# Kernel optimization log

Measured on AMD Instinct MI355X. Metric: run time of the kernel, lower is better.

The kernel has to match this reference:

```python
import jax, jax.numpy as jnp
import numpy as np

HEADS = 16
EPS = 1e-12


def setup_inputs() -> dict:
    key = jax.random.key(0)
    ks = jax.random.split(key, 5)
    B, S, H = 4, 2048, 1024
    scale = 1.0 / np.sqrt(H)
    return {
        "input": jax.random.normal(ks[0], (B, S, H), jnp.float32),
        "input_mask": jnp.zeros((B, 1, 1, S), jnp.float32),  # additive mask
        "norm_w": jnp.ones((H,), jnp.float32),
        "norm_b": jnp.zeros((H,), jnp.float32),
        "attn_qkvw": jax.random.normal(ks[1], (3 * H, H), jnp.float32) * scale,
        "attn_qkvb": jax.random.normal(ks[2], (3 * H,), jnp.float32) * 0.01,
        "attn_ow": jax.random.normal(ks[3], (H, H), jnp.float32) * scale,
    }


def reference(input, input_mask, norm_w, norm_b, attn_qkvw, attn_qkvb, attn_ow):
    B, S, H = input.shape
    d_head = H // HEADS

    # qkv_gemm: fused LayerNorm + QKV projection (pre_layer_norm path)
    mu = jnp.mean(input, axis=-1, keepdims=True)
    var = jnp.mean(jnp.square(input - mu), axis=-1, keepdims=True)
    ln = (input - mu) * jax.lax.rsqrt(var + EPS) * norm_w + norm_b
    qkv = ln @ attn_qkvw.T + attn_qkvb  # [B,S,3H]

    q, k, v = jnp.split(qkv, 3, axis=-1)  # each [B,S,H]
    key_layer, value_layer = k, v  # returned pre-transpose, as in the fused path

    qh = q.reshape(B, S, HEADS, d_head).transpose(0, 2, 1, 3)  # [B,h,S,d]
    kh = k.reshape(B, S, HEADS, d_head).transpose(0, 2, 1, 3)
    vh = v.reshape(B, S, HEADS, d_head).transpose(0, 2, 1, 3)

    # fused softmax-attention: score scale nets to 1/sqrt(d_head)
    scores = jnp.einsum("bhqd,bhkd->bhqk", qh, kh) / jnp.sqrt(
        jnp.asarray(d_head, input.dtype)) + input_mask
    p = jax.nn.softmax(scores, axis=-1)
    ctx = jnp.einsum("bhqk,bhkd->bhqd", p, vh)  # [B,h,S,d]
    context_layer = ctx.transpose(0, 2, 1, 3).reshape(B, S, H)

    # vector_matmul output projection (bias added outside this module)
    output = context_layer @ attn_ow.T
    return (output, key_layer, value_layer, context_layer)
```

## Files before the change

### kernel.cpp

```cpp
#include <hip/hip_runtime.h>
#include <cstdint>


typedef __attribute__((ext_vector_type(8))) short short8;
typedef __attribute__((ext_vector_type(4))) short short4v;
typedef __attribute__((ext_vector_type(4))) float floatx4;

#define BSH 8388608
#define PART_STRIDE 8388608
#define LOG2E 1.4426950408889634f

static __device__ __forceinline__ short f2bf(float f) {
  union { float f; uint32_t u; } v; v.f = f;
  uint32_t r = v.u + 0x7fffu + ((v.u >> 16) & 1u);
  return (short)(r >> 16);
}

typedef __attribute__((address_space(1))) void gas_t;
typedef __attribute__((address_space(3))) void las_t;
static __device__ __forceinline__ void async16(const void* g, const void* l) {
  __builtin_amdgcn_global_load_lds((gas_t*)(uintptr_t)g,
                                   (las_t*)(uint32_t)(uintptr_t)l, 16, 0, 0);
}

static __device__ __forceinline__ uint32_t cvt_pk_bf16(float a, float b) {
  uint32_t r;
  asm("v_cvt_pk_bf16_f32 %0, %1, %2" : "=v"(r) : "v"(a), "v"(b));
  return r;
}
static __device__ __forceinline__ void swap32(uint32_t& a, uint32_t& b) {
  asm("v_permlane32_swap_b32 %0, %1" : "+v"(a), "+v"(b));
}
static __device__ __forceinline__ void swap16(uint32_t& a, uint32_t& b) {
  asm("v_permlane16_swap_b32 %0, %1" : "+v"(a), "+v"(b));
}
static __device__ __forceinline__ short8 s8_from(uint32_t a, uint32_t b,
                                                 uint32_t c, uint32_t d) {
  union { uint32_t u[4]; short8 s; } t;
  t.u[0] = a; t.u[1] = b; t.u[2] = c; t.u[3] = d;
  return t.s;
}

__global__ __launch_bounds__(256) void k_convert(const float4* __restrict__ wqkv,
                                                 const float4* __restrict__ ow,
                                                 short4v* __restrict__ dq,
                                                 short4v* __restrict__ dow) {
  const int n1 = (3072 * 1024) / 4, n2 = (1024 * 1024) / 4;
  for (int i = blockIdx.x * 256 + threadIdx.x; i < n1 + n2; i += gridDim.x * 256) {
    float4 v = (i < n1) ? wqkv[i] : ow[i - n1];
    short4v s;
    s[0] = f2bf(v.x); s[1] = f2bf(v.y); s[2] = f2bf(v.z); s[3] = f2bf(v.w);
    if (i < n1) dq[i] = s; else dow[i - n1] = s;
  }
}

__global__ __launch_bounds__(256) void k_ln(const float* __restrict__ x,
                                            const float* __restrict__ w,
                                            const float* __restrict__ bb,
                                            short* __restrict__ out) {
  const int row = blockIdx.x, t = threadIdx.x;
  float4 v = ((const float4*)(x + row * 1024))[t];
  float s = v.x + v.y + v.z + v.w;
  float sq = v.x * v.x + v.y * v.y + v.z * v.z + v.w * v.w;
#pragma unroll
  for (int off = 32; off; off >>= 1) { s += __shfl_down(s, off); sq += __shfl_down(sq, off); }
  __shared__ float ls[4], lq[4];
  if ((t & 63) == 0) { ls[t >> 6] = s; lq[t >> 6] = sq; }
  __syncthreads();
  s = ls[0] + ls[1] + ls[2] + ls[3];
  sq = lq[0] + lq[1] + lq[2] + lq[3];
  float mu = s * (1.0f / 1024.0f);
  float var = sq * (1.0f / 1024.0f) - mu * mu;
  float rs = rsqrtf(fmaxf(var, 0.0f) + 1e-12f);
  float4 wv = ((const float4*)w)[t];
  float4 bv = ((const float4*)bb)[t];
  short4v o;
  o[0] = f2bf((v.x - mu) * rs * wv.x + bv.x);
  o[1] = f2bf((v.y - mu) * rs * wv.y + bv.y);
  o[2] = f2bf((v.z - mu) * rs * wv.z + bv.z);
  o[3] = f2bf((v.w - mu) * rs * wv.w + bv.w);
  ((short4v*)out)[row * 256 + t] = o;
}

template <int MODE>
__global__ __launch_bounds__(256) void k_gemm(const short* __restrict__ A,
                                              const short* __restrict__ Bm,
                                              const float* __restrict__ bias,
                                              float* __restrict__ out,
                                              short* __restrict__ qkvh,
                                              int K, int N) {
  __shared__ short As[128 * 32], Bs[128 * 32];
  const int tid = threadIdx.x, lane = tid & 63, w = tid >> 6;
  const int quad = lane >> 4, l15 = lane & 15;
  const int wr = w >> 1, wc = w & 1;
  const int m0 = blockIdx.y * 128, n0 = blockIdx.x * 128;
  floatx4 acc[4][4] = {};
  for (int k0 = 0; k0 < K; k0 += 32) {
    __syncthreads();
#pragma unroll
    for (int r = 0; r < 2; r++) {
      int pb = r * 256 + w * 64;
      int p = pb + lane;
      int row = p >> 2, c = (p & 3) ^ ((p >> 3) & 3);
      async16(&A[(m0 + row) * K + k0 + c * 8], &As[pb * 8]);
      async16(&Bm[(n0 + row) * K + k0 + c * 8], &Bs[pb * 8]);
    }
    __syncthreads();
    short8 af[4], bf[4];
#pragma unroll
    for (int i = 0; i < 4; i++) {
      int ar = wr * 64 + i * 16 + l15;
      af[i] = *(const short8*)&As[ar * 32 + ((quad ^ ((ar >> 1) & 3)) * 8)];
      int br = wc * 64 + i * 16 + l15;
      bf[i] = *(const short8*)&Bs[br * 32 + ((quad ^ ((br >> 1) & 3)) * 8)];
    }
#pragma unroll
    for (int i = 0; i < 4; i++)
#pragma unroll
      for (int j = 0; j < 4; j++)
        acc[i][j] = __builtin_amdgcn_mfma_f32_16x16x32_bf16(af[i], bf[j], acc[i][j], 0, 0, 0);
  }
  const int grB = m0 + wr * 64, gcB = n0 + wc * 64;
  const float QS = 0.125f * LOG2E;
#pragma unroll
  for (int i = 0; i < 4; i++) {
#pragma unroll
    for (int j = 0; j < 4; j++) {
      int gc = gcB + j * 16 + l15;
      if (MODE == 0) {
        float bv = bias[gc];
        int part = gc >> 10, within = gc & 1023;
        int head = within >> 6, dd = within & 63;
#pragma unroll
        for (int reg = 0; reg < 4; reg++) {
          int gr = grB + i * 16 + quad * 4 + reg;
          float val = acc[i][j][reg] + bv;
          int b_ = gr >> 11, s_ = gr & 2047;
          int hs = (b_ * 16 + head);
          if (part == 0) {
            qkvh[(hs * 2048 + s_) * 64 + dd] = f2bf(val * QS);
          } else if (part == 1) {
            qkvh[PART_STRIDE + (hs * 2048 + s_) * 64 + dd] = f2bf(val);
            out[BSH + gr * 1024 + within] = val;
          } else {
            out[2 * BSH + gr * 1024 + within] = val;
          }
        }
      } else {
#pragma unroll
        for (int reg = 0; reg < 4; reg++) {
          int gr = grB + i * 16 + quad * 4 + reg;
          out[gr * N + gc] = acc[i][j][reg];
        }
      }
    }
  }
}

__global__ __launch_bounds__(256) void k_vt(const float* __restrict__ vsrc,
                                            short* __restrict__ vt) {
  const int st = blockIdx.x, h = blockIdx.y, b = blockIdx.z;
  const int t = threadIdx.x;
  __shared__ short Ls[64 * 64];
  const int s0 = st * 64;
#pragma unroll
  for (int j = 0; j < 4; j++) {
    int flat = j * 1024 + t * 4;
    int sl = flat >> 6, d = flat & 63;
    float4 v4 = *(const float4*)&vsrc[(size_t)(b * 2048 + s0 + sl) * 1024 + h * 64 + d];
    short4v s4;
    s4[0] = f2bf(v4.x); s4[1] = f2bf(v4.y); s4[2] = f2bf(v4.z); s4[3] = f2bf(v4.w);
    *(short4v*)&Ls[sl * 64 + (((d >> 3) ^ (sl & 7)) * 8) + (d & 7)] = s4;
  }
  __syncthreads();
  const int d = t >> 2, sbase = (t & 3) * 16;
#pragma unroll
  for (int half = 0; half < 2; half++) {
    short8 o;
#pragma unroll
    for (int j = 0; j < 8; j++) {
      int s = sbase + half * 8 + j;
      o[j] = Ls[s * 64 + (((d >> 3) ^ (s & 7)) * 8) + (d & 7)];
    }
    *(short8*)&vt[(size_t)((b * 16 + h) * 64 + d) * 2048 + s0 + sbase + half * 8] = o;
  }
}

__global__ __launch_bounds__(256, 4) void k_attn(const short* __restrict__ qkvh,
                                                 const float* __restrict__ mask,
                                                 float* __restrict__ ctx_out,
                                                 short* __restrict__ ctx_bf) {
  const int bid = blockIdx.x;
  const int wid = (bid & 7) * 128 + (bid >> 3);
  const int qt = wid & 15, h = (wid >> 4) & 15, b = wid >> 8;
  const int tid = threadIdx.x, lane = tid & 63, w = tid >> 6;
  const int quad = lane >> 4, l15 = lane & 15;
  __shared__ short Ks[2][64 * 64];
  __shared__ short Vt[2][64 * 64];
  const short* qg = qkvh + (size_t)(b * 16 + h) * 2048 * 64;
  const short* kg = qg + PART_STRIDE;
  const short* vg = qkvh + 2 * PART_STRIDE + (size_t)(b * 16 + h) * 64 * 2048;
  const float* mb = mask + b * 2048;

  short8 qf[2][2];
#pragma unroll
  for (int rt = 0; rt < 2; rt++) {
    const int qr = qt * 128 + w * 32 + rt * 16 + l15;
#pragma unroll
    for (int ks = 0; ks < 2; ks++)
      qf[rt][ks] = *(const short8*)&qg[qr * 64 + ks * 32 + quad * 8];
  }

  short8 ones;
#pragma unroll
  for (int j = 0; j < 8; j++) ones[j] = (short)0x3F80;

  floatx4 accO[2][4] = {};
  floatx4 accL[2] = {};

  auto stage = [&](int kt, int bi) {
#pragma unroll
    for (int r = 0; r < 2; r++) {
      int pb = r * 256 + w * 64;
      int p = pb + lane;
      int row = p >> 3, c = (p & 7) ^ (row & 7);
      async16(&kg[(kt * 64 + row) * 64 + c * 8], &Ks[bi][pb * 8]);
      async16(&vg[row * 2048 + kt * 64 + c * 8], &Vt[bi][pb * 8]);
    }
  };
  stage(0, 0);

  for (int kt = 0; kt < 32; kt++) {
    const int cur = kt & 1;
    __syncthreads();
    if (kt + 1 < 32) stage(kt + 1, cur ^ 1);

    float mv[4][4];
#pragma unroll
    for (int nt = 0; nt < 4; nt++) {
      float4 t = *(const float4*)&mb[kt * 64 + nt * 16 + quad * 4];
      mv[nt][0] = t.x; mv[nt][1] = t.y; mv[nt][2] = t.z; mv[nt][3] = t.w;
    }

    floatx4 sc[2][4] = {};
#pragma unroll
    for (int nt = 0; nt < 4; nt++) {
      const int krow = nt * 16 + l15;
#pragma unroll
      for (int ks = 0; ks < 2; ks++) {
        short8 kf = *(const short8*)&Ks[cur][krow * 64 + (((ks * 4 + quad) ^ (krow & 7)) * 8)];
        sc[0][nt] = __builtin_amdgcn_mfma_f32_16x16x32_bf16(kf, qf[0][ks], sc[0][nt], 0, 0, 0);
        sc[1][nt] = __builtin_amdgcn_mfma_f32_16x16x32_bf16(kf, qf[1][ks], sc[1][nt], 0, 0, 0);
      }
    }

    uint32_t pa[2][2][4];
#pragma unroll
    for (int rt = 0; rt < 2; rt++) {
#pragma unroll
      for (int e = 0; e < 2; e++) {
#pragma unroll
        for (int d = 0; d < 2; d++) {
          float p0 = __builtin_amdgcn_exp2f(fmaf(mv[2 * e][2 * d], LOG2E, sc[rt][2 * e][2 * d]));
          float p1 = __builtin_amdgcn_exp2f(fmaf(mv[2 * e][2 * d + 1], LOG2E, sc[rt][2 * e][2 * d + 1]));
          float p2 = __builtin_amdgcn_exp2f(fmaf(mv[2 * e + 1][2 * d], LOG2E, sc[rt][2 * e + 1][2 * d]));
          float p3 = __builtin_amdgcn_exp2f(fmaf(mv[2 * e + 1][2 * d + 1], LOG2E, sc[rt][2 * e + 1][2 * d + 1]));
          uint32_t rE = cvt_pk_bf16(p0, p1);
          uint32_t rO = cvt_pk_bf16(p2, p3);
          swap32(rE, rO);
          swap16(rE, rO);
          pa[rt][e][d] = rE;
          pa[rt][e][2 + d] = rO;
        }
      }
    }

#pragma unroll
    for (int ks2 = 0; ks2 < 2; ks2++) {
      short8 pf0 = s8_from(pa[0][ks2][0], pa[0][ks2][1], pa[0][ks2][2], pa[0][ks2][3]);
      short8 pf1 = s8_from(pa[1][ks2][0], pa[1][ks2][1], pa[1][ks2][2], pa[1][ks2][3]);
      accL[0] = __builtin_amdgcn_mfma_f32_16x16x32_bf16(pf0, ones, accL[0], 0, 0, 0);
      accL[1] = __builtin_amdgcn_mfma_f32_16x16x32_bf16(pf1, ones, accL[1], 0, 0, 0);
#pragma unroll
      for (int nt2 = 0; nt2 < 4; nt2++) {
        const int vrow = nt2 * 16 + l15;
        short8 vf = *(const short8*)&Vt[cur][vrow * 64 + (((ks2 * 4 + quad) ^ (vrow & 7)) * 8)];
        accO[0][nt2] = __builtin_amdgcn_mfma_f32_16x16x32_bf16(pf0, vf, accO[0][nt2], 0, 0, 0);
        accO[1][nt2] = __builtin_amdgcn_mfma_f32_16x16x32_bf16(pf1, vf, accO[1][nt2], 0, 0, 0);
      }
    }
  }

#pragma unroll
  for (int rt = 0; rt < 2; rt++) {
    float inv[4];
#pragma unroll
    for (int reg = 0; reg < 4; reg++) inv[reg] = 1.0f / accL[rt][reg];
#pragma unroll
    for (int nt2 = 0; nt2 < 4; nt2++)
#pragma unroll
      for (int reg = 0; reg < 4; reg++) {
        const int qrow = qt * 128 + w * 32 + rt * 16 + quad * 4 + reg;
        const int col = h * 64 + nt2 * 16 + l15;
        const int gi = (b * 2048 + qrow) * 1024 + col;
        float val = accO[rt][nt2][reg] * inv[reg];
        ctx_out[gi] = val;
        ctx_bf[gi] = f2bf(val);
      }
  }
}

extern "C" void kernel_launch(void* const* d_in, const int* in_sizes, int n_in,
                              void* d_out, int out_size, void* d_ws, size_t ws_size,
                              hipStream_t stream) {
  const float* x    = (const float*)d_in[0];
  const float* mask = (const float*)d_in[1];
  const float* nw   = (const float*)d_in[2];
  const float* nb   = (const float*)d_in[3];
  const float* wqkv = (const float*)d_in[4];
  const float* bqkv = (const float*)d_in[5];
  const float* ow   = (const float*)d_in[6];
  float* out = (float*)d_out;
  char* ws = (char*)d_ws;

  short* lnb   = (short*)ws;
  short* wqkvb = (short*)(ws + 16777216);
  short* owb   = (short*)(ws + 23068672);
  short* qkvh  = (short*)(ws + 25165824);
  short* vt    = qkvh + 2 * (size_t)PART_STRIDE;

  k_convert<<<512, 256, 0, stream>>>((const float4*)wqkv, (const float4*)ow,
                                     (short4v*)wqkvb, (short4v*)owb);
  k_ln<<<8192, 256, 0, stream>>>(x, nw, nb, lnb);
  k_gemm<0><<<dim3(24, 64), 256, 0, stream>>>(lnb, wqkvb, bqkv, out, qkvh, 1024, 3072);
  k_vt<<<dim3(32, 16, 4), 256, 0, stream>>>(out + 2 * (size_t)BSH, vt);
  k_attn<<<1024, 256, 0, stream>>>(qkvh, mask, out + 3 * (size_t)BSH, lnb);
  k_gemm<1><<<dim3(8, 64), 256, 0, stream>>>(lnb, owb, nullptr, out, nullptr, 1024, 1024);
}
```

Measured before the change: 376.8 us.

## Double-buffer GEMM LDS tiles with 256x128 blocks and K-tile of 64

Restructures the bf16 MFMA GEMM to use 512-thread blocks covering 256x128 output tiles, a K step of 64, and double-buffered LDS so the async global-to-LDS load of the next tile overlaps MFMA work on the current one. This cuts the barrier count per K step from two to one and halves global load instructions per FLOP. It uses more LDS (96KB per block), which limits occupancy, and a single barrier per iteration makes correctness depend on the async loads having landed before the next barrier.

```diff
diff --git a/kernel.cpp b/kernel.cpp
--- a/kernel.cpp
+++ b/kernel.cpp
@@ -83,58 +83,76 @@
 }
 
 template <int MODE>
-__global__ __launch_bounds__(256) void k_gemm(const short* __restrict__ A,
-                                              const short* __restrict__ Bm,
-                                              const float* __restrict__ bias,
-                                              float* __restrict__ out,
-                                              short* __restrict__ qkvh,
-                                              int K, int N) {
-  __shared__ short As[128 * 32], Bs[128 * 32];
+__global__ __launch_bounds__(512, 2) void k_gemm(const short* __restrict__ A,
+                                                 const short* __restrict__ Bm,
+                                                 const float* __restrict__ bias,
+                                                 float* __restrict__ out,
+                                                 short* __restrict__ qkvh,
+                                                 int K, int N) {
+  __shared__ short As[2][256 * 64];
+  __shared__ short Bs[2][128 * 64];
   const int tid = threadIdx.x, lane = tid & 63, w = tid >> 6;
   const int quad = lane >> 4, l15 = lane & 15;
-  const int wr = w >> 1, wc = w & 1;
-  const int m0 = blockIdx.y * 128, n0 = blockIdx.x * 128;
+  const int wm = w >> 1, wn = w & 1;
+  const int m0 = blockIdx.y * 256, n0 = blockIdx.x * 128;
+  const int srow = tid >> 3;
+  const int sc8 = (tid & 7) ^ (srow & 7);
+
   floatx4 acc[4][4] = {};
-  for (int k0 = 0; k0 < K; k0 += 32) {
+
+  auto stage = [&](int kt, int bi) {
+    const short* asrc = &A[(size_t)(m0 + srow) * K + kt * 64 + sc8 * 8];
+#pragma unroll
+    for (int u = 0; u < 4; u++)
+      async16(asrc + (size_t)u * 64 * K, &As[bi][u * 4096 + tid * 8]);
+    const short* bsrc = &Bm[(size_t)(n0 + srow) * K + kt * 64 + sc8 * 8];
+#pragma unroll
+    for (int u = 0; u < 2; u++)
+      async16(bsrc + (size_t)u * 64 * K, &Bs[bi][u * 4096 + tid * 8]);
+  };
+
+  stage(0, 0);
+  const int NT = K >> 6;
+  for (int kt = 0; kt < NT; kt++) {
+    const int cur = kt & 1;
     __syncthreads();
-#pragma unroll
-    for (int r = 0; r < 2; r++) {
-      int pb = r * 256 + w * 64;
-      int p = pb + lane;
-      int row = p >> 2, c = (p & 3) ^ ((p >> 3) & 3);
-      async16(&A[(m0 + row) * K + k0 + c * 8], &As[pb * 8]);
-      async16(&Bm[(n0 + row) * K + k0 + c * 8], &Bs[pb * 8]);
-    }
-    __syncthreads();
-    short8 af[4], bf[4];
-#pragma unroll
-    for (int i = 0; i < 4; i++) {
-      int ar = wr * 64 + i * 16 + l15;
-      af[i] = *(const short8*)&As[ar * 32 + ((quad ^ ((ar >> 1) & 3)) * 8)];
-      int br = wc * 64 + i * 16 + l15;
-      bf[i] = *(const short8*)&Bs[br * 32 + ((quad ^ ((br >> 1) & 3)) * 8)];
-    }
-#pragma unroll
-    for (int i = 0; i < 4; i++)
-#pragma unroll
-      for (int j = 0; j < 4; j++)
-        acc[i][j] = __builtin_amdgcn_mfma_f32_16x16x32_bf16(af[i], bf[j], acc[i][j], 0, 0, 0);
-  }
-  const int grB = m0 + wr * 64, gcB = n0 + wc * 64;
+    if (kt + 1 < NT) stage(kt + 1, cur ^ 1);
+#pragma unroll
+    for (int ks = 0; ks < 2; ks++) {
+      short8 af[4], bf[4];
+#pragma unroll
+      for (int m = 0; m < 4; m++) {
+        const int r = wm * 64 + m * 16 + l15;
+        af[m] = *(const short8*)&As[cur][r * 64 + (((ks * 4 + quad) ^ (r & 7)) * 8)];
+      }
+#pragma unroll
+      for (int n = 0; n < 4; n++) {
+        const int r = wn * 64 + n * 16 + l15;
+        bf[n] = *(const short8*)&Bs[cur][r * 64 + (((ks * 4 + quad) ^ (r & 7)) * 8)];
+      }
+#pragma unroll
+      for (int m = 0; m < 4; m++)
+#pragma unroll
+        for (int n = 0; n < 4; n++)
+          acc[m][n] = __builtin_amdgcn_mfma_f32_16x16x32_bf16(af[m], bf[n], acc[m][n], 0, 0, 0);
+    }
+  }
+
+  const int grB = m0 + wm * 64, gcB = n0 + wn * 64;
   const float QS = 0.125f * LOG2E;
 #pragma unroll
-  for (int i = 0; i < 4; i++) {
-#pragma unroll
-    for (int j = 0; j < 4; j++) {
-      int gc = gcB + j * 16 + l15;
+  for (int m = 0; m < 4; m++) {
+#pragma unroll
+    for (int n = 0; n < 4; n++) {
+      int gc = gcB + n * 16 + l15;
       if (MODE == 0) {
         float bv = bias[gc];
         int part = gc >> 10, within = gc & 1023;
         int head = within >> 6, dd = within & 63;
 #pragma unroll
         for (int reg = 0; reg < 4; reg++) {
-          int gr = grB + i * 16 + quad * 4 + reg;
-          float val = acc[i][j][reg] + bv;
+          int gr = grB + m * 16 + quad * 4 + reg;
+          float val = acc[m][n][reg] + bv;
           int b_ = gr >> 11, s_ = gr & 2047;
           int hs = (b_ * 16 + head);
           if (part == 0) {
@@ -149,8 +167,8 @@
       } else {
 #pragma unroll
         for (int reg = 0; reg < 4; reg++) {
-          int gr = grB + i * 16 + quad * 4 + reg;
-          out[gr * N + gc] = acc[i][j][reg];
+          int gr = grB + m * 16 + quad * 4 + reg;
+          out[gr * N + gc] = acc[m][n][reg];
         }
       }
     }
@@ -332,8 +350,8 @@
   k_convert<<<512, 256, 0, stream>>>((const float4*)wqkv, (const float4*)ow,
                                      (short4v*)wqkvb, (short4v*)owb);
   k_ln<<<8192, 256, 0, stream>>>(x, nw, nb, lnb);
-  k_gemm<0><<<dim3(24, 64), 256, 0, stream>>>(lnb, wqkvb, bqkv, out, qkvh, 1024, 3072);
+  k_gemm<0><<<dim3(24, 32), 512, 0, stream>>>(lnb, wqkvb, bqkv, out, qkvh, 1024, 3072);
   k_vt<<<dim3(32, 16, 4), 256, 0, stream>>>(out + 2 * (size_t)BSH, vt);
   k_attn<<<1024, 256, 0, stream>>>(qkvh, mask, out + 3 * (size_t)BSH, lnb);
-  k_gemm<1><<<dim3(8, 64), 256, 0, stream>>>(lnb, owb, nullptr, out, nullptr, 1024, 1024);
-}
+  k_gemm<1><<<dim3(8, 32), 512, 0, stream>>>(lnb, owb, nullptr, out, nullptr, 1024, 1024);
+}
```

Measured after the change: 350.4 us. -7.0%, faster.
